# Optimization experiments

Hardware: AMD Instinct MI355X
Metric: run time of the kernel (lower is better)

Reference implementation:

```python
import jax, jax.numpy as jnp
import numpy as np

N_NODES = 100000
N_EDGES = 1600000
IN_CH, HID1, HID2, HID3, OUT_CH = 128, 64, 64, 256, 64


def gcn_conv(x, W, b, src, dst, n_nodes):
    """PyG GCNConv: linear transform, add self-loops, symmetric-normalized aggregation."""
    h = x @ W  # [N, d_out]
    # degree at target nodes, counting the self-loop (+1)
    deg = jnp.zeros((n_nodes,), dtype=h.dtype).at[dst].add(1.0) + 1.0
    dinv = jax.lax.rsqrt(deg)  # deg >= 1, safe
    norm = dinv[src] * dinv[dst]  # [E]
    # scatter-add normalized messages from src to dst
    agg = jnp.zeros_like(h).at[dst].add(h[src] * norm[:, None])
    # self-loop contribution: norm_ii = dinv[i]^2
    agg = agg + h * (dinv * dinv)[:, None]
    return agg + b


def setup_inputs() -> dict:
    key = jax.random.key(0)
    ks = jax.random.split(key, 8)
    x = jax.random.normal(ks[0], (N_NODES, IN_CH), dtype=jnp.float32)
    edge_index = jax.random.randint(ks[1], (2, N_EDGES), 0, N_NODES, dtype=jnp.int64)
    def glorot(k, fan_in, fan_out):
        s = jnp.sqrt(6.0 / (fan_in + fan_out)).astype(jnp.float32)
        return jax.random.uniform(k, (fan_in, fan_out), jnp.float32, -s, s)
    return {
        "x": x,
        "edge_index": edge_index,
        "W1": glorot(ks[2], IN_CH, HID1), "b1": jnp.zeros((HID1,), jnp.float32),
        "W2": glorot(ks[3], HID1, HID2), "b2": jnp.zeros((HID2,), jnp.float32),
        "W3": glorot(ks[4], HID2, HID3), "b3": jnp.zeros((HID3,), jnp.float32),
        "W4": glorot(ks[5], HID3, OUT_CH), "b4": jnp.zeros((OUT_CH,), jnp.float32),
    }


def reference(x, edge_index, W1, b1, W2, b2, W3, b3, W4, b4):
    src, dst = edge_index[0], edge_index[1]
    n = x.shape[0]
    h = jax.nn.relu(gcn_conv(x, W1, b1, src, dst, n))
    h = jax.nn.relu(gcn_conv(h, W2, b2, src, dst, n))
    h = h @ W3 + b3  # hidden Linear (no activation, per original forward)
    h = h @ W4 + b4  # output Linear
    return jax.nn.log_softmax(h, axis=-1)
```

## Files before the change

kernel.cpp:

```cpp
#include <hip/hip_runtime.h>
#include <hip/hip_bf16.h>
#include <math.h>

#define NNODES 100000
#define NEDGES 1600000
#define NB 782
#define PB 256
#define EPB 6250
#define SCAN_N (NB * PB)
#define CAP 4608

typedef __bf16 bf16x8 __attribute__((ext_vector_type(8)));
typedef float f32x4 __attribute__((ext_vector_type(4)));

static __device__ inline unsigned short f2bf(float f) {
    __hip_bfloat16 h = __float2bfloat16(f);
    return *reinterpret_cast<unsigned short*>(&h);
}

static __device__ inline float bf2f(unsigned short u) {
    unsigned int x = ((unsigned int)u) << 16;
    return __builtin_bit_cast(float, x);
}


__global__ __launch_bounds__(256) void hist_kernel(const int* __restrict__ dst,
                                                   int* __restrict__ histg) {
    __shared__ int h[NB];
    int tid = threadIdx.x, blk = blockIdx.x;
    for (int b = tid; b < NB; b += 256) h[b] = 0;
    __syncthreads();
    int base = blk * EPB;
    for (int i = base + tid; i < base + EPB; i += 256)
        atomicAdd(&h[dst[i] >> 7], 1);
    __syncthreads();
    for (int b = tid; b < NB; b += 256) histg[b * PB + blk] = h[b];
}


__global__ __launch_bounds__(256) void scan1_kernel(const int* __restrict__ cnt,
                                                    int* __restrict__ off,
                                                    int* __restrict__ bsum, int n) {
    __shared__ int tmp[256];
    int tid = threadIdx.x;
    int t4 = blockIdx.x * 1024 + tid * 4;
    int v0 = (t4 + 0 < n) ? cnt[t4 + 0] : 0;
    int v1 = (t4 + 1 < n) ? cnt[t4 + 1] : 0;
    int v2 = (t4 + 2 < n) ? cnt[t4 + 2] : 0;
    int v3 = (t4 + 3 < n) ? cnt[t4 + 3] : 0;
    int ssum = v0 + v1 + v2 + v3;
    tmp[tid] = ssum;
    __syncthreads();
    for (int d = 1; d < 256; d <<= 1) {
        int x = (tid >= d) ? tmp[tid - d] : 0;
        __syncthreads();
        tmp[tid] += x;
        __syncthreads();
    }
    int run = tmp[tid] - ssum;
    if (t4 + 0 < n) off[t4 + 0] = run; run += v0;
    if (t4 + 1 < n) off[t4 + 1] = run; run += v1;
    if (t4 + 2 < n) off[t4 + 2] = run; run += v2;
    if (t4 + 3 < n) off[t4 + 3] = run;
    if (tid == 255) bsum[blockIdx.x] = tmp[255];
}

__global__ __launch_bounds__(256) void scan2_kernel(const int* __restrict__ bsum,
                                                    int* __restrict__ bsum_ex, int nb) {
    __shared__ int tmp[256];
    int tid = threadIdx.x;
    int v = (tid < nb) ? bsum[tid] : 0;
    tmp[tid] = v;
    __syncthreads();
    for (int d = 1; d < 256; d <<= 1) {
        int x = (tid >= d) ? tmp[tid - d] : 0;
        __syncthreads();
        tmp[tid] += x;
        __syncthreads();
    }
    bsum_ex[tid] = tmp[tid] - v;
}

__global__ __launch_bounds__(256) void scan3t_kernel(const int* __restrict__ part_scan,
                                                     const int* __restrict__ bsum_ex,
                                                     const int* __restrict__ histg,
                                                     int* __restrict__ gbaseT,
                                                     int* __restrict__ cntT, int n) {
    int i = blockIdx.x * 256 + threadIdx.x;
    if (i < n) {
        int v = part_scan[i] + bsum_ex[i >> 10];
        int b = i >> 8, blk = i & 255;
        gbaseT[blk * NB + b] = v;
        cntT[blk * NB + b] = histg[i];
    }
}


__global__ __launch_bounds__(256) void part_kernel(const int* __restrict__ src,
                                                   const int* __restrict__ dst,
                                                   const int* __restrict__ gbaseT,
                                                   const int* __restrict__ cntT,
                                                   unsigned int* __restrict__ part) {
    __shared__ unsigned int sorted[EPB];
    __shared__ int gaddr[EPB];
    __shared__ int gcol[NB];
    __shared__ int base_l[NB];
    __shared__ int cur[NB];
    __shared__ int tmp[256];
    int tid = threadIdx.x, blk = blockIdx.x;
    for (int b = tid; b < NB; b += 256) {
        gcol[b] = gbaseT[blk * NB + b];
        base_l[b] = cntT[blk * NB + b];
        cur[b] = 0;
    }
    __syncthreads();
    int t4 = tid * 4;
    int v0 = (t4 + 0 < NB) ? base_l[t4 + 0] : 0;
    int v1 = (t4 + 1 < NB) ? base_l[t4 + 1] : 0;
    int v2 = (t4 + 2 < NB) ? base_l[t4 + 2] : 0;
    int v3 = (t4 + 3 < NB) ? base_l[t4 + 3] : 0;
    int ssum = v0 + v1 + v2 + v3;
    tmp[tid] = ssum;
    __syncthreads();
    for (int d = 1; d < 256; d <<= 1) {
        int x = (tid >= d) ? tmp[tid - d] : 0;
        __syncthreads();
        tmp[tid] += x;
        __syncthreads();
    }
    int run = tmp[tid] - ssum;
    if (t4 + 0 < NB) base_l[t4 + 0] = run; run += v0;
    if (t4 + 1 < NB) base_l[t4 + 1] = run; run += v1;
    if (t4 + 2 < NB) base_l[t4 + 2] = run; run += v2;
    if (t4 + 3 < NB) base_l[t4 + 3] = run;
    __syncthreads();
    int base = blk * EPB;
    for (int i = base + tid; i < base + EPB; i += 256) {
        int s = src[i], d = dst[i];
        int bkt = d >> 7;
        int r = atomicAdd(&cur[bkt], 1);
        int pos = base_l[bkt] + r;
        sorted[pos] = ((unsigned int)(d & 127) << 17) | (unsigned int)s;
        gaddr[pos] = gcol[bkt] + r;
    }
    __syncthreads();
    for (int i = tid; i < EPB; i += 256)
        part[gaddr[i]] = sorted[i];
}


__global__ __launch_bounds__(256) void csr_kernel(const unsigned int* __restrict__ part,
                                                  const int* __restrict__ gbaseT,
                                                  int* __restrict__ csr,
                                                  int* __restrict__ cnt_g,
                                                  int* __restrict__ off_g,
                                                  float* __restrict__ dinv_g, int n) {
    __shared__ unsigned int stage[CAP];
    __shared__ int hist2[128];
    __shared__ int sc[128];
    __shared__ int excl[128];
    __shared__ int cur2[128];
    int tid = threadIdx.x, b = blockIdx.x;
    int S = gbaseT[b];
    int T = (b == NB - 1) ? NEDGES : gbaseT[b + 1];
    int len = T - S;
    bool fit = (len <= CAP);
    if (tid < 128) { hist2[tid] = 0; cur2[tid] = 0; }
    __syncthreads();
    for (int i = tid; i < len; i += 256) {
        unsigned int p = part[S + i];
        if (fit) stage[i] = p;
        atomicAdd(&hist2[p >> 17], 1);
    }
    __syncthreads();
    if (tid < 128) sc[tid] = hist2[tid];
    __syncthreads();
    for (int d = 1; d < 128; d <<= 1) {
        int x = 0;
        if (tid < 128 && tid >= d) x = sc[tid - d];
        __syncthreads();
        if (tid < 128) sc[tid] += x;
        __syncthreads();
    }
    if (tid < 128) {
        int c = hist2[tid];
        int ex = sc[tid] - c;
        excl[tid] = ex;
        int node = b * 128 + tid;
        if (node < n) {
            cnt_g[node] = c;
            off_g[node] = S + ex;
            dinv_g[node] = rsqrtf((float)c + 1.0f);
        }
    }
    __syncthreads();
    for (int i = tid; i < len; i += 256) {
        unsigned int p = fit ? stage[i] : part[S + i];
        int dl = p >> 17;
        int s = (int)(p & 0x1FFFFu);
        int r = atomicAdd(&cur2[dl], 1);
        csr[S + excl[dl] + r] = s;
    }
}


static __device__ inline int packidx64(int k, int ch) {
    int s = k >> 5, r5 = k & 31, q = r5 >> 3, ii = r5 & 7;
    int t = ch >> 4, lo = ch & 15;
    int lane = q * 16 + lo;
    return ((t * 2 + s) * 64 + lane) * 8 + ii;
}

__global__ __launch_bounds__(256) void prep_kernel(const float* __restrict__ W1,
                                                   const float* __restrict__ W2,
                                                   const float* __restrict__ W3,
                                                   const float* __restrict__ W4,
                                                   const float* __restrict__ b3,
                                                   const float* __restrict__ b4,
                                                   unsigned short* __restrict__ Wp1,
                                                   unsigned short* __restrict__ Wp2,
                                                   unsigned short* __restrict__ Wp34,
                                                   float* __restrict__ b34,
                                                   unsigned short* __restrict__ hp) {
    int blk = blockIdx.x, tid = threadIdx.x;
    if (blk < 32) {
        int idx = blk * 256 + tid;
        int i = idx & 7, rest = idx >> 3;
        int lane = rest & 63; rest >>= 6;
        int s = rest % 4, t = rest / 4;
        int k = s * 32 + (lane >> 4) * 8 + i;
        int ch = t * 16 + (lane & 15);
        Wp1[idx] = f2bf(W1[k * 64 + ch]);
    } else if (blk < 48) {
        int idx = (blk - 32) * 256 + tid;
        int i = idx & 7, rest = idx >> 3;
        int lane = rest & 63; rest >>= 6;
        int s = rest % 2, t = rest / 2;
        int k = s * 32 + (lane >> 4) * 8 + i;
        int ch = t * 16 + (lane & 15);
        Wp2[idx] = f2bf(W2[k * 64 + ch]);
    } else if (blk == 48) {
        if (tid < 64) hp[(size_t)NNODES * 64 + tid] = 0;
    } else if (blk < 65) {
        int i = (blk - 49) * 4 + (tid >> 6);
        int j = tid & 63;
        float a = 0.f;
        for (int k = 0; k < 256; ++k) a = fmaf(W3[i * 256 + k], W4[k * 64 + j], a);
        Wp34[packidx64(i, j)] = f2bf(a);
    } else {
        if (tid < 64) {
            int j = tid;
            float a = b4[j];
            for (int k = 0; k < 256; ++k) a = fmaf(b3[k], W4[k * 64 + j], a);
            b34[j] = a;
        }
    }
}


template <int K, bool LSM, bool F32IN>
__global__ __launch_bounds__(256) void gemm_mfma_kernel(const unsigned short* __restrict__ Xb,
                                                        const float* __restrict__ Xf,
                                                        const unsigned short* __restrict__ Wp,
                                                        const float* __restrict__ bias,
                                                        const float* __restrict__ dinv,
                                                        unsigned short* __restrict__ outb,
                                                        float* __restrict__ outf, int n) {
    constexpr int S = K / 32;
    int w = threadIdx.x >> 6, lane = threadIdx.x & 63;
    int q = lane >> 4, lo = lane & 15;
    int base = blockIdx.x * 64 + w * 16;
    int nodeA = base + lo;
    int na = nodeA < n ? nodeA : 0;

    f32x4 acc[4] = {};
#pragma unroll
    for (int s = 0; s < S; ++s) {
        bf16x8 a;
        if (F32IN) {
            const float* xr = Xf + (size_t)na * K + q * 8 + s * 32;
            float4 u = *(const float4*)(xr);
            float4 v = *(const float4*)(xr + 4);
            a[0] = (__bf16)u.x; a[1] = (__bf16)u.y; a[2] = (__bf16)u.z; a[3] = (__bf16)u.w;
            a[4] = (__bf16)v.x; a[5] = (__bf16)v.y; a[6] = (__bf16)v.z; a[7] = (__bf16)v.w;
        } else {
            a = *(const bf16x8*)(Xb + (size_t)na * K + q * 8 + s * 32);
        }
#pragma unroll
        for (int t = 0; t < 4; ++t) {
            bf16x8 b = *(const bf16x8*)(Wp + ((size_t)(t * S + s) * 64 + lane) * 8);
            acc[t] = __builtin_amdgcn_mfma_f32_16x16x32_bf16(a, b, acc[t], 0, 0, 0);
        }
    }

    if (!LSM) {
#pragma unroll
        for (int r = 0; r < 4; ++r) {
            int node = base + q * 4 + r;
            if (node < n) {
                float di = dinv[node];
#pragma unroll
                for (int t = 0; t < 4; ++t)
                    outb[(size_t)node * 64 + t * 16 + lo] = f2bf(acc[t][r] * di);
            }
        }
    } else {
#pragma unroll
        for (int r = 0; r < 4; ++r) {
            int node = base + q * 4 + r;
            float v0 = acc[0][r] + bias[0 * 16 + lo];
            float v1 = acc[1][r] + bias[1 * 16 + lo];
            float v2 = acc[2][r] + bias[2 * 16 + lo];
            float v3 = acc[3][r] + bias[3 * 16 + lo];
            float mx = fmaxf(fmaxf(v0, v1), fmaxf(v2, v3));
            for (int d = 1; d < 16; d <<= 1) mx = fmaxf(mx, __shfl_xor(mx, d));
            float sm = __expf(v0 - mx) + __expf(v1 - mx) + __expf(v2 - mx) + __expf(v3 - mx);
            for (int d = 1; d < 16; d <<= 1) sm += __shfl_xor(sm, d);
            float lse = mx + __logf(sm);
            if (node < n) {
                outf[(size_t)node * 64 + 0 * 16 + lo] = v0 - lse;
                outf[(size_t)node * 64 + 1 * 16 + lo] = v1 - lse;
                outf[(size_t)node * 64 + 2 * 16 + lo] = v2 - lse;
                outf[(size_t)node * 64 + 3 * 16 + lo] = v3 - lse;
            }
        }
    }
}


__global__ __launch_bounds__(256) void aggregate_kernel(const unsigned short* __restrict__ hp,
                                                        const int* __restrict__ csr,
                                                        const int* __restrict__ off,
                                                        const int* __restrict__ cnt,
                                                        const float* __restrict__ dinv,
                                                        const float* __restrict__ bias,
                                                        unsigned short* __restrict__ out, int n) {
    int wid = (blockIdx.x * 256 + threadIdx.x) >> 6;
    int lane = threadIdx.x & 63;
    if (wid >= n) return;
    int g = lane >> 3;
    int c8 = (lane & 7) * 8;

    int s = off[wid];
    int c = cnt[wid];

    int idx = n;
    if (lane < c) idx = csr[s + lane];
    else if (lane == c) idx = wid;

    int m = (c <= 63) ? c + 1 : 64;
    int steps = (m + 7) >> 3;

    float acc0[8] = {}, acc1[8] = {};
    int it = 0;
    for (; it + 2 <= steps; it += 2) {
        int sa = __shfl(idx, it * 8 + g);
        int sb = __shfl(idx, it * 8 + 8 + g);
        bf16x8 va = *(const bf16x8*)(hp + (size_t)sa * 64 + c8);
        bf16x8 vb = *(const bf16x8*)(hp + (size_t)sb * 64 + c8);
#pragma unroll
        for (int j = 0; j < 8; ++j) { acc0[j] += (float)va[j]; acc1[j] += (float)vb[j]; }
    }
    if (it < steps) {
        int sa = __shfl(idx, it * 8 + g);
        bf16x8 va = *(const bf16x8*)(hp + (size_t)sa * 64 + c8);
#pragma unroll
        for (int j = 0; j < 8; ++j) acc0[j] += (float)va[j];
    }

    if (c > 63) {
        if (g == 0) {
            bf16x8 v = *(const bf16x8*)(hp + (size_t)wid * 64 + c8);
#pragma unroll
            for (int j = 0; j < 8; ++j) acc1[j] += (float)v[j];
        }
        for (int jj = 64 + g; jj < c; jj += 8) {
            int srcn = csr[s + jj];
            bf16x8 v = *(const bf16x8*)(hp + (size_t)srcn * 64 + c8);
#pragma unroll
            for (int j = 0; j < 8; ++j) acc0[j] += (float)v[j];
        }
    }

#pragma unroll
    for (int j = 0; j < 8; ++j) acc0[j] += acc1[j];

#pragma unroll
    for (int d = 8; d < 64; d <<= 1)
#pragma unroll
        for (int j = 0; j < 8; ++j) acc0[j] += __shfl_xor(acc0[j], d);

    if (lane < 8) {
        float di = dinv[wid];
        float4 bv0 = *(const float4*)(bias + c8);
        float4 bv1 = *(const float4*)(bias + c8 + 4);
        float bb[8] = {bv0.x, bv0.y, bv0.z, bv0.w, bv1.x, bv1.y, bv1.z, bv1.w};
        unsigned short ov[8];
#pragma unroll
        for (int j = 0; j < 8; ++j)
            ov[j] = f2bf(fmaxf(fmaf(acc0[j], di, bb[j]), 0.f));
        *(ushort4*)(out + (size_t)wid * 64 + c8) = make_ushort4(ov[0], ov[1], ov[2], ov[3]);
        *(ushort4*)(out + (size_t)wid * 64 + c8 + 4) = make_ushort4(ov[4], ov[5], ov[6], ov[7]);
    }
}


extern "C" void kernel_launch(void* const* d_in, const int* in_sizes, int n_in,
                              void* d_out, int out_size, void* d_ws, size_t ws_size,
                              hipStream_t stream) {
    const float* x  = (const float*)d_in[0];
    const int*   ei = (const int*)d_in[1];
    const float* W1 = (const float*)d_in[2];
    const float* b1 = (const float*)d_in[3];
    const float* W2 = (const float*)d_in[4];
    const float* b2 = (const float*)d_in[5];
    const float* W3 = (const float*)d_in[6];
    const float* b3 = (const float*)d_in[7];
    const float* W4 = (const float*)d_in[8];
    const float* b4 = (const float*)d_in[9];
    float* outp = (float*)d_out;

    const int N = NNODES;
    const int E = NEDGES;
    const int* srcp = ei;
    const int* dstp = ei + E;

    char* w = (char*)d_ws;
    size_t o = 0;
    auto alloc = [&](size_t bytes) { size_t r = o; o = (o + bytes + 255) & ~(size_t)255; return r; };
    size_t cnt_off   = alloc((size_t)N * 4);
    size_t off_off   = alloc((size_t)N * 4);
    size_t dinv_off  = alloc((size_t)N * 4);
    size_t histg_off = alloc((size_t)SCAN_N * 4);
    size_t gscan_off = alloc((size_t)SCAN_N * 4);
    size_t gbT_off   = alloc((size_t)SCAN_N * 4);
    size_t cntT_off  = alloc((size_t)SCAN_N * 4);
    size_t bs_off    = alloc(256 * 4);
    size_t bse_off   = alloc(256 * 4);
    size_t part_off  = alloc((size_t)E * 4);
    size_t csr_off   = alloc((size_t)E * 4);
    size_t hp_off    = alloc((size_t)(N + 1) * 64 * 2);
    size_t abf_off   = alloc((size_t)N * 64 * 2);
    size_t wp1_off   = alloc(128 * 64 * 2);
    size_t wp2_off   = alloc(64 * 64 * 2);
    size_t wp34_off  = alloc(64 * 64 * 2);
    size_t b34_off   = alloc(64 * 4);

    int*            cnt   = (int*)(w + cnt_off);
    int*            off   = (int*)(w + off_off);
    float*          dinv  = (float*)(w + dinv_off);
    int*            histg = (int*)(w + histg_off);
    int*            gscan = (int*)(w + gscan_off);
    int*            gbT   = (int*)(w + gbT_off);
    int*            cntT  = (int*)(w + cntT_off);
    int*            bs    = (int*)(w + bs_off);
    int*            bse   = (int*)(w + bse_off);
    unsigned int*   part  = (unsigned int*)(w + part_off);
    int*            csr   = (int*)(w + csr_off);
    unsigned short* hp    = (unsigned short*)(w + hp_off);
    unsigned short* abf   = (unsigned short*)(w + abf_off);
    unsigned short* Wp1   = (unsigned short*)(w + wp1_off);
    unsigned short* Wp2   = (unsigned short*)(w + wp2_off);
    unsigned short* Wp34  = (unsigned short*)(w + wp34_off);
    float*          b34   = (float*)(w + b34_off);

    const int sb = (SCAN_N + 1023) / 1024;
    const int s3b = (SCAN_N + 255) / 256;

    hist_kernel<<<PB, 256, 0, stream>>>(dstp, histg);
    scan1_kernel<<<sb, 256, 0, stream>>>(histg, gscan, bs, SCAN_N);
    scan2_kernel<<<1, 256, 0, stream>>>(bs, bse, sb);
    scan3t_kernel<<<s3b, 256, 0, stream>>>(gscan, bse, histg, gbT, cntT, SCAN_N);
    part_kernel<<<PB, 256, 0, stream>>>(srcp, dstp, gbT, cntT, part);
    csr_kernel<<<NB, 256, 0, stream>>>(part, gbT, csr, cnt, off, dinv, N);

    prep_kernel<<<66, 256, 0, stream>>>(W1, W2, W3, W4, b3, b4, Wp1, Wp2, Wp34, b34, hp);

    const int gb = (N + 63) / 64;
    const int ab = (N + 3) / 4;

    gemm_mfma_kernel<128, false, true><<<gb, 256, 0, stream>>>(nullptr, x, Wp1, nullptr, dinv, hp, nullptr, N);
    aggregate_kernel<<<ab, 256, 0, stream>>>(hp, csr, off, cnt, dinv, b1, abf, N);
    gemm_mfma_kernel<64, false, false><<<gb, 256, 0, stream>>>(abf, nullptr, Wp2, nullptr, dinv, hp, nullptr, N);
    aggregate_kernel<<<ab, 256, 0, stream>>>(hp, csr, off, cnt, dinv, b2, abf, N);
    gemm_mfma_kernel<64, true, false><<<gb, 256, 0, stream>>>(abf, nullptr, Wp34, b34, nullptr, nullptr, outp, N);
}
```

Baseline: 277.3 us.

## Aggregate each node with eight lanes instead of a full wavefront

The aggregation kernel now assigns 8 threads per node, each covering 8 channels, instead of a 64-lane wavefront that split neighbors across lane groups and then reduced them with cross-lane shuffles. Each thread walks the CSR neighbor list serially, prefetching the next two indices, and converts bf16 to float with bit shifts. This removes the shuffle reduction and the idle lanes for low-degree nodes (average degree is 16), at the cost of serial latency per neighbor and less memory-level parallelism per node.

```diff
diff --git a/kernel.cpp b/kernel.cpp
--- a/kernel.cpp
+++ b/kernel.cpp
@@ -12,15 +12,11 @@
 
 typedef __bf16 bf16x8 __attribute__((ext_vector_type(8)));
 typedef float f32x4 __attribute__((ext_vector_type(4)));
+typedef unsigned int u32x4 __attribute__((ext_vector_type(4)));
 
 static __device__ inline unsigned short f2bf(float f) {
     __hip_bfloat16 h = __float2bfloat16(f);
     return *reinterpret_cast<unsigned short*>(&h);
-}
-
-static __device__ inline float bf2f(unsigned short u) {
-    unsigned int x = ((unsigned int)u) << 16;
-    return __builtin_bit_cast(float, x);
 }
 
 
@@ -335,73 +331,65 @@
                                                         const float* __restrict__ dinv,
                                                         const float* __restrict__ bias,
                                                         unsigned short* __restrict__ out, int n) {
-    int wid = (blockIdx.x * 256 + threadIdx.x) >> 6;
-    int lane = threadIdx.x & 63;
-    if (wid >= n) return;
-    int g = lane >> 3;
-    int c8 = (lane & 7) * 8;
-
-    int s = off[wid];
-    int c = cnt[wid];
-
-    int idx = n;
-    if (lane < c) idx = csr[s + lane];
-    else if (lane == c) idx = wid;
-
-    int m = (c <= 63) ? c + 1 : 64;
-    int steps = (m + 7) >> 3;
-
-    float acc0[8] = {}, acc1[8] = {};
-    int it = 0;
-    for (; it + 2 <= steps; it += 2) {
-        int sa = __shfl(idx, it * 8 + g);
-        int sb = __shfl(idx, it * 8 + 8 + g);
-        bf16x8 va = *(const bf16x8*)(hp + (size_t)sa * 64 + c8);
-        bf16x8 vb = *(const bf16x8*)(hp + (size_t)sb * 64 + c8);
-#pragma unroll
-        for (int j = 0; j < 8; ++j) { acc0[j] += (float)va[j]; acc1[j] += (float)vb[j]; }
-    }
-    if (it < steps) {
-        int sa = __shfl(idx, it * 8 + g);
-        bf16x8 va = *(const bf16x8*)(hp + (size_t)sa * 64 + c8);
-#pragma unroll
-        for (int j = 0; j < 8; ++j) acc0[j] += (float)va[j];
-    }
-
-    if (c > 63) {
-        if (g == 0) {
-            bf16x8 v = *(const bf16x8*)(hp + (size_t)wid * 64 + c8);
-#pragma unroll
-            for (int j = 0; j < 8; ++j) acc1[j] += (float)v[j];
-        }
-        for (int jj = 64 + g; jj < c; jj += 8) {
-            int srcn = csr[s + jj];
-            bf16x8 v = *(const bf16x8*)(hp + (size_t)srcn * 64 + c8);
-#pragma unroll
-            for (int j = 0; j < 8; ++j) acc0[j] += (float)v[j];
-        }
-    }
-
-#pragma unroll
-    for (int j = 0; j < 8; ++j) acc0[j] += acc1[j];
-
-#pragma unroll
-    for (int d = 8; d < 64; d <<= 1)
-#pragma unroll
-        for (int j = 0; j < 8; ++j) acc0[j] += __shfl_xor(acc0[j], d);
-
-    if (lane < 8) {
-        float di = dinv[wid];
-        float4 bv0 = *(const float4*)(bias + c8);
-        float4 bv1 = *(const float4*)(bias + c8 + 4);
-        float bb[8] = {bv0.x, bv0.y, bv0.z, bv0.w, bv1.x, bv1.y, bv1.z, bv1.w};
-        unsigned short ov[8];
-#pragma unroll
-        for (int j = 0; j < 8; ++j)
-            ov[j] = f2bf(fmaxf(fmaf(acc0[j], di, bb[j]), 0.f));
-        *(ushort4*)(out + (size_t)wid * 64 + c8) = make_ushort4(ov[0], ov[1], ov[2], ov[3]);
-        *(ushort4*)(out + (size_t)wid * 64 + c8 + 4) = make_ushort4(ov[4], ov[5], ov[6], ov[7]);
-    }
+    int node = (blockIdx.x * 256 + threadIdx.x) >> 3;
+    int cl = threadIdx.x & 7;
+    if (node >= n) return;
+    int c8 = cl * 8;
+    int s = off[node];
+    int c = cnt[node];
+    const int* cp = csr + s;
+
+    float acc0[8];
+    float acc1[8] = {};
+    {
+        bf16x8 sv = *(const bf16x8*)(hp + (size_t)node * 64 + c8);
+        u32x4 su = __builtin_bit_cast(u32x4, sv);
+#pragma unroll
+        for (int k = 0; k < 4; ++k) {
+            acc0[2 * k]     = __builtin_bit_cast(float, su[k] << 16);
+            acc0[2 * k + 1] = __builtin_bit_cast(float, su[k] & 0xFFFF0000u);
+        }
+    }
+
+    int n0 = 0, n1 = 0;
+    if (c > 0) n0 = cp[0];
+    if (c > 1) n1 = cp[1];
+    int j = 0;
+    for (; j + 2 <= c; j += 2) {
+        bf16x8 va = *(const bf16x8*)(hp + (size_t)n0 * 64 + c8);
+        bf16x8 vb = *(const bf16x8*)(hp + (size_t)n1 * 64 + c8);
+        if (j + 3 < c)      { n0 = cp[j + 2]; n1 = cp[j + 3]; }
+        else if (j + 2 < c) { n0 = cp[j + 2]; }
+        u32x4 ua = __builtin_bit_cast(u32x4, va);
+        u32x4 ub = __builtin_bit_cast(u32x4, vb);
+#pragma unroll
+        for (int k = 0; k < 4; ++k) {
+            acc0[2 * k]     += __builtin_bit_cast(float, ua[k] << 16);
+            acc0[2 * k + 1] += __builtin_bit_cast(float, ua[k] & 0xFFFF0000u);
+            acc1[2 * k]     += __builtin_bit_cast(float, ub[k] << 16);
+            acc1[2 * k + 1] += __builtin_bit_cast(float, ub[k] & 0xFFFF0000u);
+        }
+    }
+    if (j < c) {
+        bf16x8 va = *(const bf16x8*)(hp + (size_t)n0 * 64 + c8);
+        u32x4 ua = __builtin_bit_cast(u32x4, va);
+#pragma unroll
+        for (int k = 0; k < 4; ++k) {
+            acc0[2 * k]     += __builtin_bit_cast(float, ua[k] << 16);
+            acc0[2 * k + 1] += __builtin_bit_cast(float, ua[k] & 0xFFFF0000u);
+        }
+    }
+
+    float di = dinv[node];
+    float4 bv0 = *(const float4*)(bias + c8);
+    float4 bv1 = *(const float4*)(bias + c8 + 4);
+    float bb[8] = {bv0.x, bv0.y, bv0.z, bv0.w, bv1.x, bv1.y, bv1.z, bv1.w};
+    unsigned short ov[8];
+#pragma unroll
+    for (int k = 0; k < 8; ++k)
+        ov[k] = f2bf(fmaxf(fmaf(acc0[k] + acc1[k], di, bb[k]), 0.f));
+    *(ushort4*)(out + (size_t)node * 64 + c8)     = make_ushort4(ov[0], ov[1], ov[2], ov[3]);
+    *(ushort4*)(out + (size_t)node * 64 + c8 + 4) = make_ushort4(ov[4], ov[5], ov[6], ov[7]);
 }
 
 
@@ -477,7 +465,7 @@
     prep_kernel<<<66, 256, 0, stream>>>(W1, W2, W3, W4, b3, b4, Wp1, Wp2, Wp34, b34, hp);
 
     const int gb = (N + 63) / 64;
-    const int ab = (N + 3) / 4;
+    const int ab = (N * 8 + 255) / 256;
 
     gemm_mfma_kernel<128, false, true><<<gb, 256, 0, stream>>>(nullptr, x, Wp1, nullptr, dinv, hp, nullptr, N);
     aggregate_kernel<<<ab, 256, 0, stream>>>(hp, csr, off, cnt, dinv, b1, abf, N);
```

After: 256.1 us. 7.6% less time.
